# Kernel tuning notes

Hardware: AMD Instinct MI355X
Metric: run time of the kernel (lower is better)

The kernel has to match this reference:

```python
import jax, jax.numpy as jnp
import numpy as np

BATCH, SEQ, DIM = 256, 80, 1024
HEADS = 8
HID = 4 * DIM
EPS = 1e-5


def _ln(x, g, b):
    mu = jnp.mean(x, axis=-1, keepdims=True)
    var = jnp.mean((x - mu) ** 2, axis=-1, keepdims=True)
    return (x - mu) * jax.lax.rsqrt(var + EPS) * g + b


def setup_inputs() -> dict:
    key = jax.random.key(0)
    ks = jax.random.split(key, 8)
    w = lambda k, shape: jax.random.normal(k, shape, dtype=jnp.float32) * 0.02
    return {
        "x": jax.random.normal(ks[0], (BATCH, SEQ, DIM), dtype=jnp.float32),
        "Wq": w(ks[1], (DIM, DIM)),
        "Wk": w(ks[2], (DIM, DIM)),
        "Wv": w(ks[3], (DIM, DIM)),
        "bias_table": w(ks[4], (2 * SEQ - 1, HEADS)),
        "to_out_g": jnp.ones((DIM,), jnp.float32),
        "to_out_b": jnp.zeros((DIM,), jnp.float32),
        "ln1_g": jnp.ones((DIM,), jnp.float32),
        "ln1_b": jnp.zeros((DIM,), jnp.float32),
        "ln2_g": jnp.ones((DIM,), jnp.float32),
        "ln2_b": jnp.zeros((DIM,), jnp.float32),
        "fc1_w": w(ks[5], (DIM, HID)),
        "fc1_b": jnp.zeros((HID,), jnp.float32),
        "fc2_w": w(ks[6], (HID, DIM)),
        "fc2_b": jnp.zeros((DIM,), jnp.float32),
    }


def reference(x, Wq, Wk, Wv, bias_table, to_out_g, to_out_b,
              ln1_g, ln1_b, ln2_g, ln2_b, fc1_w, fc1_b, fc2_w, fc2_b):
    B, S, E = x.shape
    H = HEADS
    D = E // H
    scale = E ** (-0.5)  # NOTE: full emb_size scale, faithful to source

    q = (x @ Wq).reshape(B, S, H, D).transpose(0, 2, 1, 3)  # bhsd
    k = (x @ Wk).reshape(B, S, H, D).transpose(0, 2, 1, 3)
    v = (x @ Wv).reshape(B, S, H, D).transpose(0, 2, 1, 3)

    attn = jnp.einsum('bhqd,bhkd->bhqk', q, k) * scale
    attn = jax.nn.softmax(attn, axis=-1)

    # relative bias added AFTER softmax (non-standard, faithful)
    idx = jnp.arange(S)[:, None] - jnp.arange(S)[None, :] + (S - 1)  # [S,S] in [0,2S-2]
    bias = bias_table[idx].transpose(2, 0, 1)  # (H, S, S)
    attn = attn + bias[None]

    out = jnp.einsum('bhqk,bhkd->bhqd', attn, v)
    out = out.transpose(0, 2, 1, 3).reshape(B, S, E)
    out = _ln(out, to_out_g, to_out_b)  # LayerNorm inside attention (to_out)

    x = _ln(x + out, ln1_g, ln1_b)      # post-norm residual 1
    h = jax.nn.gelu(x @ fc1_w + fc1_b, approximate=False)  # torch nn.GELU exact
    ff = h @ fc2_w + fc2_b
    return _ln(x + ff, ln2_g, ln2_b)    # post-norm residual 2
```

## Files before the change

### kernel.cpp

```cpp
#include <hip/hip_runtime.h>
#include <stdint.h>

#define BATCH 256
#define SEQ   80
#define DIM   1024
#define HEADS 8
#define HDIM  128
#define HID   4096
#define NTOK  (BATCH * SEQ)

typedef unsigned short u16;
using short8_t = __attribute__((ext_vector_type(8))) short;
using f32x4    = __attribute__((ext_vector_type(4))) float;

__device__ __forceinline__ u16 f2bf(float f) {
  unsigned u = __float_as_uint(f);
  u += 0x7fffu + ((u >> 16) & 1u);
  return (u16)(u >> 16);
}
__device__ __forceinline__ float bf2f(u16 u) {
  return __uint_as_float(((unsigned)u) << 16);
}

__device__ __forceinline__ float gelu_exact(float v) {
  return 0.5f * v * (1.0f + erff(v * 0.70710678118654752f));
}

#define GLD16(gp, lp)                                                   \
  __builtin_amdgcn_global_load_lds(                                     \
      (__attribute__((address_space(1))) void*)(void*)(gp),             \
      (__attribute__((address_space(3))) void*)(void*)(lp), 16, 0, 0)

__global__ __launch_bounds__(256) void cast_bf16_kernel(
    const float* __restrict__ in, u16* __restrict__ out, int n4) {
  int i = blockIdx.x * 256 + threadIdx.x;
  int stride = gridDim.x * 256;
  for (; i < n4; i += stride) {
    float4 v = ((const float4*)in)[i];
    uint2 o;
    o.x = (unsigned)f2bf(v.x) | ((unsigned)f2bf(v.y) << 16);
    o.y = (unsigned)f2bf(v.z) | ((unsigned)f2bf(v.w) << 16);
    ((uint2*)out)[i] = o;
  }
}

__global__ __launch_bounds__(256) void transpose_cast_kernel(
    const float* __restrict__ in, u16* __restrict__ out, int R, int C) {
  __shared__ float tile[32][33];
  int c0 = blockIdx.x * 32, r0 = blockIdx.y * 32;
  for (int k = 0; k < 4; k++) {
    int i = threadIdx.y + k * 8;
    tile[i][threadIdx.x] = in[(size_t)(r0 + i) * C + c0 + threadIdx.x];
  }
  __syncthreads();
  for (int k = 0; k < 4; k++) {
    int i = threadIdx.y + k * 8;
    out[(size_t)(c0 + i) * R + r0 + threadIdx.x] = f2bf(tile[threadIdx.x][i]);
  }
}

template <int EPI>
__global__ __launch_bounds__(512, 2) void gemm256(
    const u16* __restrict__ A, const u16* __restrict__ Bt,
    const float* __restrict__ bias, u16* __restrict__ outp,
    int M, int N, int K, int ntn) {
  __shared__ __align__(16) u16 lds[65536];

  const int tid  = threadIdx.x;
  const int lane = tid & 63, wave = tid >> 6;
  const int wm = wave >> 2, wn = wave & 3;
  const int lo = lane & 15, hi = lane >> 4;

  const int nwg = gridDim.x;
  {
  }
  int q8 = nwg >> 3, r8 = nwg & 7;
  int xcd = blockIdx.x & 7, off = blockIdx.x >> 3;
  int swz = (xcd < r8 ? xcd * (q8 + 1) : r8 * (q8 + 1) + (xcd - r8) * q8) + off;
  const int bn = swz % ntn;
  const int bm = swz / ntn;
  const size_t arow0 = (size_t)bm * 256;
  const size_t bcol0 = (size_t)bn * 256;

  const int prow = tid >> 2;
  const int lb = (tid & 3) ^ ((tid >> 3) & 3);
  const u16* srcA = A + (arow0 + prow) * K + lb * 8;
  const u16* srcB = Bt + (bcol0 + prow) * K + lb * 8;
  const size_t jstep = 128 * (size_t)K;

  u16* ldsA0 = lds + wave * 512;
  u16* ldsA1 = lds + 4096 + wave * 512;
  u16* ldsB0 = lds + 8192 + wave * 512;
  u16* ldsB1 = lds + 12288 + wave * 512;

  const int blk = hi ^ ((lo >> 1) & 3);
  const int abase = (wm * 128 + lo) * 32 + blk * 8;
  const int bbase = 8192 + (wn * 64 + lo) * 32 + blk * 8;

  f32x4 acc[8][4] = {};
  const int NT = K >> 5;

#pragma unroll
  for (int tt = 0; tt < 3; ++tt) {
    const u16* sa = srcA + (size_t)tt * 32;
    const u16* sb = srcB + (size_t)tt * 32;
    GLD16(sa, ldsA0 + tt * 16384);
    GLD16(sa + jstep, ldsA1 + tt * 16384);
    GLD16(sb, ldsB0 + tt * 16384);
    GLD16(sb + jstep, ldsB1 + tt * 16384);
  }
  asm volatile("s_waitcnt vmcnt(8)" ::: "memory");
  asm volatile("s_barrier" ::: "memory");

#define PHASES(T, DO_STAGE, VMASM)                                             \
  do {                                                                         \
    const int bufb = ((T) & 3) * 16384;                                        \
    short8_t a0[4], b0[4], a1[4];                                              \
    _Pragma("unroll") for (int m = 0; m < 4; ++m)                              \
        a0[m] = *(const short8_t*)&lds[bufb + abase + m * 512];                \
    _Pragma("unroll") for (int n = 0; n < 4; ++n)                              \
        b0[n] = *(const short8_t*)&lds[bufb + bbase + n * 512];                \
    if (DO_STAGE) {                                                            \
      const u16* sa = srcA + (size_t)((T) + 3) * 32;                           \
      GLD16(sa, ldsA0 + (((T) + 3) & 3) * 16384);                              \
      GLD16(sa + jstep, ldsA1 + (((T) + 3) & 3) * 16384);                      \
    }                                                                          \
    asm volatile("s_barrier" ::: "memory");                                    \
    __builtin_amdgcn_s_setprio(1);                                             \
    _Pragma("unroll") for (int m = 0; m < 4; ++m)                              \
        _Pragma("unroll") for (int n = 0; n < 4; ++n)                          \
            acc[m][n] = __builtin_amdgcn_mfma_f32_16x16x32_bf16(               \
                a0[m], b0[n], acc[m][n], 0, 0, 0);                             \
    __builtin_amdgcn_s_setprio(0);                                             \
    asm volatile("s_barrier" ::: "memory");                                    \
    _Pragma("unroll") for (int m = 0; m < 4; ++m)                              \
        a1[m] = *(const short8_t*)&lds[bufb + abase + (4 + m) * 512];          \
    if (DO_STAGE) {                                                            \
      const u16* sb = srcB + (size_t)((T) + 3) * 32;                           \
      GLD16(sb, ldsB0 + (((T) + 3) & 3) * 16384);                              \
      GLD16(sb + jstep, ldsB1 + (((T) + 3) & 3) * 16384);                      \
    }                                                                          \
    asm volatile("s_barrier" ::: "memory");                                    \
    __builtin_amdgcn_s_setprio(1);                                             \
    _Pragma("unroll") for (int m = 0; m < 4; ++m)                              \
        _Pragma("unroll") for (int n = 0; n < 4; ++n)                          \
            acc[4 + m][n] = __builtin_amdgcn_mfma_f32_16x16x32_bf16(           \
                a1[m], b0[n], acc[4 + m][n], 0, 0, 0);                         \
    __builtin_amdgcn_s_setprio(0);                                             \
    asm volatile(VMASM ::: "memory");                                          \
    asm volatile("s_barrier" ::: "memory");                                    \
  } while (0)

  for (int t = 0; t < NT - 3; ++t) PHASES(t, 1, "s_waitcnt vmcnt(8)");
  PHASES(NT - 3, 0, "s_waitcnt vmcnt(4)");
  PHASES(NT - 2, 0, "s_waitcnt vmcnt(0)");
  PHASES(NT - 1, 0, "");
#undef PHASES

  const size_t crow0 = arow0 + wm * 128;
  const int ccol0 = (int)bcol0 + wn * 64;
#pragma unroll
  for (int n = 0; n < 4; ++n) {
    int col = ccol0 + n * 16 + lo;
    float bv = 0.f;
    if constexpr (EPI != 0) bv = bias[col];
#pragma unroll
    for (int m = 0; m < 8; ++m) {
#pragma unroll
      for (int j = 0; j < 4; ++j) {
        size_t row = crow0 + m * 16 + hi * 4 + j;
        float v = acc[m][n][j] + bv;
        if constexpr (EPI == 1) v = gelu_exact(v);
        outp[row * N + col] = f2bf(v);
      }
    }
  }
}

__global__ __launch_bounds__(64) void attn_kernel(
    const u16* __restrict__ QKV, const float* __restrict__ bias_table,
    u16* __restrict__ attnout) {
  __shared__ __align__(16) u16 Kt[80 * 128];
  __shared__ __align__(16) u16 Vt[96 * 128];
  __shared__ float bias_l[159];

  const int bh = blockIdx.x;
  const int b = bh >> 3, h = bh & 7;
  const int lane = threadIdx.x, lo = lane & 15, hi = lane >> 4;
  const size_t tokbase = (size_t)b * SEQ * 3072;
  const u16* Qg = QKV + tokbase + h * HDIM;
  const u16* Kg = QKV + tokbase + 1024 + h * HDIM;
  const u16* Vg = QKV + tokbase + 2048 + h * HDIM;

#pragma unroll
  for (int i = 0; i < 20; i++) {
    int flat = i * 64 + lane;
    int row = flat >> 4;
    int col = (flat & 15) * 8;
    GLD16(Kg + (size_t)row * 3072 + col, &Kt[i * 512]);
    GLD16(Vg + (size_t)row * 3072 + col, &Vt[i * 512]);
  }
  for (int i = lane; i < 16 * 128; i += 64) Vt[80 * 128 + i] = 0;
  for (int i = lane; i < 159; i += 64) bias_l[i] = bias_table[i * 8 + h];
  asm volatile("s_waitcnt vmcnt(0)" ::: "memory");
  __syncthreads();

  f32x4 sa[5][5] = {};
#pragma unroll
  for (int ks = 0; ks < 4; ks++) {
    short8_t ak[5], bq[5];
#pragma unroll
    for (int m = 0; m < 5; m++)
      ak[m] = *(const short8_t*)&Kt[(m * 16 + lo) * 128 + ks * 32 + hi * 8];
#pragma unroll
    for (int n = 0; n < 5; n++)
      bq[n] = *(const short8_t*)(Qg + (size_t)(n * 16 + lo) * 3072 + ks * 32 + hi * 8);
#pragma unroll
    for (int m = 0; m < 5; m++)
#pragma unroll
      for (int n = 0; n < 5; n++)
        sa[m][n] = __builtin_amdgcn_mfma_f32_16x16x32_bf16(ak[m], bq[n], sa[m][n], 0, 0, 0);
  }
  __syncthreads();

  u16* p_lds = Kt;
  for (int i = lane; i < 80 * 16; i += 64) {
    int q = i >> 4, c = 80 + (i & 15);
    p_lds[q * 104 + c] = 0;
  }
  const float scale = 0.03125f;
#pragma unroll
  for (int n = 0; n < 5; n++) {
    float mx = -1e30f;
#pragma unroll
    for (int m = 0; m < 5; m++)
#pragma unroll
      for (int j = 0; j < 4; j++) {
        sa[m][n][j] *= scale;
        mx = fmaxf(mx, sa[m][n][j]);
      }
    mx = fmaxf(mx, __shfl_xor(mx, 16));
    mx = fmaxf(mx, __shfl_xor(mx, 32));
    float sm = 0.f;
#pragma unroll
    for (int m = 0; m < 5; m++)
#pragma unroll
      for (int j = 0; j < 4; j++) {
        float e = __expf(sa[m][n][j] - mx);
        sa[m][n][j] = e;
        sm += e;
      }
    sm += __shfl_xor(sm, 16);
    sm += __shfl_xor(sm, 32);
    float inv = 1.0f / sm;
    int q = n * 16 + lo;
#pragma unroll
    for (int m = 0; m < 5; m++)
#pragma unroll
      for (int j = 0; j < 4; j++) {
        int key = m * 16 + hi * 4 + j;
        float pv = sa[m][n][j] * inv + bias_l[q - key + 79];
        p_lds[q * 104 + key] = f2bf(pv);
      }
  }
  __syncthreads();

#pragma unroll
  for (int half = 0; half < 2; half++) {
    f32x4 oa[5][4] = {};
#pragma unroll
    for (int ks = 0; ks < 3; ks++) {
      short8_t ap[5];
#pragma unroll
      for (int m = 0; m < 5; m++)
        ap[m] = *(const short8_t*)&p_lds[(m * 16 + lo) * 104 + ks * 32 + hi * 8];
      short8_t bv[4];
#pragma unroll
      for (int nd = 0; nd < 4; nd++) {
        int d = (half * 4 + nd) * 16 + lo;
        short8_t tt;
#pragma unroll
        for (int j = 0; j < 8; j++)
          tt[j] = (short)Vt[(ks * 32 + hi * 8 + j) * 128 + d];
        bv[nd] = tt;
      }
#pragma unroll
      for (int m = 0; m < 5; m++)
#pragma unroll
        for (int nd = 0; nd < 4; nd++)
          oa[m][nd] = __builtin_amdgcn_mfma_f32_16x16x32_bf16(ap[m], bv[nd], oa[m][nd], 0, 0, 0);
    }
#pragma unroll
    for (int m = 0; m < 5; m++)
#pragma unroll
      for (int nd = 0; nd < 4; nd++)
#pragma unroll
        for (int j = 0; j < 4; j++) {
          int q = m * 16 + hi * 4 + j;
          int d = (half * 4 + nd) * 16 + lo;
          attnout[((size_t)b * SEQ + q) * DIM + h * HDIM + d] = f2bf(oa[m][nd][j]);
        }
  }
}

__device__ __forceinline__ void block_reduce2(float& a, float& b, float* sbuf) {
#pragma unroll
  for (int m = 1; m < 64; m <<= 1) {
    a += __shfl_xor(a, m);
    b += __shfl_xor(b, m);
  }
  int w = threadIdx.x >> 6;
  if ((threadIdx.x & 63) == 0) { sbuf[w * 2] = a; sbuf[w * 2 + 1] = b; }
  __syncthreads();
  a = sbuf[0] + sbuf[2] + sbuf[4] + sbuf[6];
  b = sbuf[1] + sbuf[3] + sbuf[5] + sbuf[7];
  __syncthreads();
}

__global__ __launch_bounds__(256) void fuse1_kernel(
    const u16* __restrict__ attnout, const float* __restrict__ x,
    const float* __restrict__ og, const float* __restrict__ ob,
    const float* __restrict__ g1, const float* __restrict__ b1,
    u16* __restrict__ x1b) {
  __shared__ float sbuf[8];
  const size_t base = (size_t)blockIdx.x * DIM;
  float a[4], r[4];
  float s0 = 0.f, s1 = 0.f;
#pragma unroll
  for (int i = 0; i < 4; i++) {
    int idx = threadIdx.x + i * 256;
    a[i] = bf2f(attnout[base + idx]);
    s0 += a[i];
    s1 += a[i] * a[i];
  }
  block_reduce2(s0, s1, sbuf);
  float mu = s0 * (1.f / DIM);
  float rstd = rsqrtf(s1 * (1.f / DIM) - mu * mu + 1e-5f);
  float t0 = 0.f, t1 = 0.f;
#pragma unroll
  for (int i = 0; i < 4; i++) {
    int idx = threadIdx.x + i * 256;
    float o = (a[i] - mu) * rstd * og[idx] + ob[idx];
    r[i] = x[base + idx] + o;
    t0 += r[i];
    t1 += r[i] * r[i];
  }
  block_reduce2(t0, t1, sbuf);
  float mu2 = t0 * (1.f / DIM);
  float rstd2 = rsqrtf(t1 * (1.f / DIM) - mu2 * mu2 + 1e-5f);
#pragma unroll
  for (int i = 0; i < 4; i++) {
    int idx = threadIdx.x + i * 256;
    x1b[base + idx] = f2bf((r[i] - mu2) * rstd2 * g1[idx] + b1[idx]);
  }
}

__global__ __launch_bounds__(256) void fuse2_kernel(
    const u16* __restrict__ x1b, const u16* __restrict__ ff,
    const float* __restrict__ g2, const float* __restrict__ b2,
    float* __restrict__ out) {
  __shared__ float sbuf[8];
  const size_t base = (size_t)blockIdx.x * DIM;
  float r[4];
  float s0 = 0.f, s1 = 0.f;
#pragma unroll
  for (int i = 0; i < 4; i++) {
    int idx = threadIdx.x + i * 256;
    r[i] = bf2f(x1b[base + idx]) + bf2f(ff[base + idx]);
    s0 += r[i];
    s1 += r[i] * r[i];
  }
  block_reduce2(s0, s1, sbuf);
  float mu = s0 * (1.f / DIM);
  float rstd = rsqrtf(s1 * (1.f / DIM) - mu * mu + 1e-5f);
#pragma unroll
  for (int i = 0; i < 4; i++) {
    int idx = threadIdx.x + i * 256;
    out[base + idx] = (r[i] - mu) * rstd * g2[idx] + b2[idx];
  }
}

extern "C" void kernel_launch(void* const* d_in, const int* in_sizes, int n_in,
                              void* d_out, int out_size, void* d_ws, size_t ws_size,
                              hipStream_t stream) {
  const float* x        = (const float*)d_in[0];
  const float* Wq       = (const float*)d_in[1];
  const float* Wk       = (const float*)d_in[2];
  const float* Wv       = (const float*)d_in[3];
  const float* bias_tab = (const float*)d_in[4];
  const float* og       = (const float*)d_in[5];
  const float* ob       = (const float*)d_in[6];
  const float* g1       = (const float*)d_in[7];
  const float* b1       = (const float*)d_in[8];
  const float* g2       = (const float*)d_in[9];
  const float* b2       = (const float*)d_in[10];
  const float* fc1w     = (const float*)d_in[11];
  const float* fc1b     = (const float*)d_in[12];
  const float* fc2w     = (const float*)d_in[13];
  const float* fc2b     = (const float*)d_in[14];

  char* ws = (char*)d_ws;
  u16* wqkvT = (u16*)(ws + 0);
  u16* fc1T  = (u16*)(ws + 6291456ull);
  u16* fc2T  = (u16*)(ws + 14680064ull);
  u16* pbuf  = (u16*)(ws + 23068672ull);
  u16* qbuf  = (u16*)(ws + 65011712ull);
  char* cbuf = ws + 106954752ull;
  size_t cavail = ws_size > 106954752ull ? ws_size - 106954752ull : 0;

  int cb = 1;
  while (cb < 16 && (size_t)(BATCH / cb) * SEQ * 3072 * 2 > cavail) cb <<= 1;
  int cf = 1;
  while (cf < 16 && (size_t)(NTOK / cf) * HID * 2 > cavail) cf <<= 1;

  dim3 tb(32, 8);
  cast_bf16_kernel<<<2048, 256, 0, stream>>>(x, qbuf, NTOK * DIM / 4);
  transpose_cast_kernel<<<dim3(32, 32), tb, 0, stream>>>(Wq, wqkvT, 1024, 1024);
  transpose_cast_kernel<<<dim3(32, 32), tb, 0, stream>>>(Wk, wqkvT + 1024 * 1024, 1024, 1024);
  transpose_cast_kernel<<<dim3(32, 32), tb, 0, stream>>>(Wv, wqkvT + 2 * 1024 * 1024, 1024, 1024);
  transpose_cast_kernel<<<dim3(128, 32), tb, 0, stream>>>(fc1w, fc1T, 1024, 4096);
  transpose_cast_kernel<<<dim3(32, 128), tb, 0, stream>>>(fc2w, fc2T, 4096, 1024);

  {
    const int nb = BATCH / cb;
    const int rows = nb * SEQ;
    u16* qkvc = (u16*)cbuf;
    const int nwg = (rows / 256) * (3072 / 256);
    for (int c = 0; c < cb; ++c) {
      const u16* xb_c = qbuf + (size_t)c * rows * DIM;
      gemm256<0><<<nwg, 512, 0, stream>>>(xb_c, wqkvT, nullptr, qkvc,
                                          rows, 3072, 1024, 3072 / 256);
      attn_kernel<<<nb * HEADS, 64, 0, stream>>>(
          qkvc, bias_tab, pbuf + (size_t)c * rows * DIM);
    }
  }

  fuse1_kernel<<<NTOK, 256, 0, stream>>>(pbuf, x, og, ob, g1, b1, qbuf);

  {
    const int rows = NTOK / cf;
    u16* hc = (u16*)cbuf;
    const int nwg1 = (rows / 256) * (HID / 256);
    const int nwg2 = (rows / 256) * (DIM / 256);
    for (int c = 0; c < cf; ++c) {
      gemm256<1><<<nwg1, 512, 0, stream>>>(qbuf + (size_t)c * rows * DIM, fc1T,
                                           fc1b, hc, rows, HID, 1024, HID / 256);
      gemm256<2><<<nwg2, 512, 0, stream>>>(hc, fc2T, fc2b,
                                           pbuf + (size_t)c * rows * DIM,
                                           rows, 1024, HID, DIM / 256);
    }
  }

  fuse2_kernel<<<NTOK, 256, 0, stream>>>(qbuf, pbuf, g2, b2, (float*)d_out);
}
```

Measured before the change: 818.0 us.

## Switch GEMM to 32x32x16 MFMA, single barrier per K-step, LDS-staged epilogue

```diff
diff --git a/kernel.cpp b/kernel.cpp
--- a/kernel.cpp
+++ b/kernel.cpp
@@ -12,6 +12,7 @@
 typedef unsigned short u16;
 using short8_t = __attribute__((ext_vector_type(8))) short;
 using f32x4    = __attribute__((ext_vector_type(4))) float;
+using f32x16   = __attribute__((ext_vector_type(16))) float;
 
 __device__ __forceinline__ u16 f2bf(float f) {
   unsigned u = __float_as_uint(f);
@@ -69,11 +70,9 @@
   const int tid  = threadIdx.x;
   const int lane = tid & 63, wave = tid >> 6;
   const int wm = wave >> 2, wn = wave & 3;
-  const int lo = lane & 15, hi = lane >> 4;
+  const int l31 = lane & 31, khalf = lane >> 5;
 
   const int nwg = gridDim.x;
-  {
-  }
   int q8 = nwg >> 3, r8 = nwg & 7;
   int xcd = blockIdx.x & 7, off = blockIdx.x >> 3;
   int swz = (xcd < r8 ? xcd * (q8 + 1) : r8 * (q8 + 1) + (xcd - r8) * q8) + off;
@@ -88,92 +87,86 @@
   const u16* srcB = Bt + (bcol0 + prow) * K + lb * 8;
   const size_t jstep = 128 * (size_t)K;
 
-  u16* ldsA0 = lds + wave * 512;
-  u16* ldsA1 = lds + 4096 + wave * 512;
-  u16* ldsB0 = lds + 8192 + wave * 512;
-  u16* ldsB1 = lds + 12288 + wave * 512;
-
-  const int blk = hi ^ ((lo >> 1) & 3);
-  const int abase = (wm * 128 + lo) * 32 + blk * 8;
-  const int bbase = 8192 + (wn * 64 + lo) * 32 + blk * 8;
-
-  f32x4 acc[8][4] = {};
+  const int ar = wm * 128 + l31;
+  const int ab0 = ar * 32 + ((khalf ^ ((ar >> 1) & 3)) << 3);
+  const int bc = wn * 64 + l31;
+  const int bb0 = 8192 + bc * 32 + ((khalf ^ ((bc >> 1) & 3)) << 3);
+
+  f32x16 acc[4][2] = {};
   const int NT = K >> 5;
 
-#pragma unroll
-  for (int tt = 0; tt < 3; ++tt) {
-    const u16* sa = srcA + (size_t)tt * 32;
-    const u16* sb = srcB + (size_t)tt * 32;
-    GLD16(sa, ldsA0 + tt * 16384);
-    GLD16(sa + jstep, ldsA1 + tt * 16384);
-    GLD16(sb, ldsB0 + tt * 16384);
-    GLD16(sb + jstep, ldsB1 + tt * 16384);
-  }
+#define STAGE(u)                                                           \
+  do {                                                                     \
+    const u16* sa_ = srcA + (size_t)(u) * 32;                              \
+    const u16* sb_ = srcB + (size_t)(u) * 32;                              \
+    const int so_ = ((u) & 3) * 16384;                                     \
+    GLD16(sa_, lds + so_ + wave * 512);                                    \
+    GLD16(sa_ + jstep, lds + so_ + 4096 + wave * 512);                     \
+    GLD16(sb_, lds + so_ + 8192 + wave * 512);                             \
+    GLD16(sb_ + jstep, lds + so_ + 12288 + wave * 512);                    \
+  } while (0)
+
+#define ITER(t, DO_STAGE, VMASM)                                           \
+  do {                                                                     \
+    const int bo_ = ((t) & 3) * 16384;                                     \
+    short8_t af[4][2], bf[2][2];                                           \
+    _Pragma("unroll") for (int mi = 0; mi < 4; ++mi) {                     \
+      af[mi][0] = *(const short8_t*)&lds[(bo_ + ab0) + mi * 1024];         \
+      af[mi][1] = *(const short8_t*)&lds[((bo_ + ab0) ^ 16) + mi * 1024];  \
+    }                                                                      \
+    _Pragma("unroll") for (int ni = 0; ni < 2; ++ni) {                     \
+      bf[ni][0] = *(const short8_t*)&lds[(bo_ + bb0) + ni * 1024];         \
+      bf[ni][1] = *(const short8_t*)&lds[((bo_ + bb0) ^ 16) + ni * 1024];  \
+    }                                                                      \
+    if (DO_STAGE) STAGE((t) + 3);                                          \
+    __builtin_amdgcn_s_setprio(1);                                         \
+    _Pragma("unroll") for (int ks = 0; ks < 2; ++ks)                       \
+    _Pragma("unroll") for (int mi = 0; mi < 4; ++mi)                       \
+    _Pragma("unroll") for (int ni = 0; ni < 2; ++ni)                       \
+        acc[mi][ni] = __builtin_amdgcn_mfma_f32_32x32x16_bf16(             \
+            af[mi][ks], bf[ni][ks], acc[mi][ni], 0, 0, 0);                 \
+    __builtin_amdgcn_s_setprio(0);                                         \
+    asm volatile(VMASM ::: "memory");                                      \
+    asm volatile("s_barrier" ::: "memory");                                \
+  } while (0)
+
+#pragma unroll
+  for (int u = 0; u < 3; ++u) STAGE(u);
   asm volatile("s_waitcnt vmcnt(8)" ::: "memory");
   asm volatile("s_barrier" ::: "memory");
 
-#define PHASES(T, DO_STAGE, VMASM)                                             \
-  do {                                                                         \
-    const int bufb = ((T) & 3) * 16384;                                        \
-    short8_t a0[4], b0[4], a1[4];                                              \
-    _Pragma("unroll") for (int m = 0; m < 4; ++m)                              \
-        a0[m] = *(const short8_t*)&lds[bufb + abase + m * 512];                \
-    _Pragma("unroll") for (int n = 0; n < 4; ++n)                              \
-        b0[n] = *(const short8_t*)&lds[bufb + bbase + n * 512];                \
-    if (DO_STAGE) {                                                            \
-      const u16* sa = srcA + (size_t)((T) + 3) * 32;                           \
-      GLD16(sa, ldsA0 + (((T) + 3) & 3) * 16384);                              \
-      GLD16(sa + jstep, ldsA1 + (((T) + 3) & 3) * 16384);                      \
-    }                                                                          \
-    asm volatile("s_barrier" ::: "memory");                                    \
-    __builtin_amdgcn_s_setprio(1);                                             \
-    _Pragma("unroll") for (int m = 0; m < 4; ++m)                              \
-        _Pragma("unroll") for (int n = 0; n < 4; ++n)                          \
-            acc[m][n] = __builtin_amdgcn_mfma_f32_16x16x32_bf16(               \
-                a0[m], b0[n], acc[m][n], 0, 0, 0);                             \
-    __builtin_amdgcn_s_setprio(0);                                             \
-    asm volatile("s_barrier" ::: "memory");                                    \
-    _Pragma("unroll") for (int m = 0; m < 4; ++m)                              \
-        a1[m] = *(const short8_t*)&lds[bufb + abase + (4 + m) * 512];          \
-    if (DO_STAGE) {                                                            \
-      const u16* sb = srcB + (size_t)((T) + 3) * 32;                           \
-      GLD16(sb, ldsB0 + (((T) + 3) & 3) * 16384);                              \
-      GLD16(sb + jstep, ldsB1 + (((T) + 3) & 3) * 16384);                      \
-    }                                                                          \
-    asm volatile("s_barrier" ::: "memory");                                    \
-    __builtin_amdgcn_s_setprio(1);                                             \
-    _Pragma("unroll") for (int m = 0; m < 4; ++m)                              \
-        _Pragma("unroll") for (int n = 0; n < 4; ++n)                          \
-            acc[4 + m][n] = __builtin_amdgcn_mfma_f32_16x16x32_bf16(           \
-                a1[m], b0[n], acc[4 + m][n], 0, 0, 0);                         \
-    __builtin_amdgcn_s_setprio(0);                                             \
-    asm volatile(VMASM ::: "memory");                                          \
-    asm volatile("s_barrier" ::: "memory");                                    \
-  } while (0)
-
-  for (int t = 0; t < NT - 3; ++t) PHASES(t, 1, "s_waitcnt vmcnt(8)");
-  PHASES(NT - 3, 0, "s_waitcnt vmcnt(4)");
-  PHASES(NT - 2, 0, "s_waitcnt vmcnt(0)");
-  PHASES(NT - 1, 0, "");
-#undef PHASES
-
-  const size_t crow0 = arow0 + wm * 128;
-  const int ccol0 = (int)bcol0 + wn * 64;
-#pragma unroll
-  for (int n = 0; n < 4; ++n) {
-    int col = ccol0 + n * 16 + lo;
+#pragma unroll 4
+  for (int t = 0; t < NT - 3; ++t) ITER(t, 1, "s_waitcnt vmcnt(8)");
+  ITER(NT - 3, 0, "s_waitcnt vmcnt(4)");
+  ITER(NT - 2, 0, "s_waitcnt vmcnt(0)");
+  ITER(NT - 1, 0, "");
+#undef ITER
+#undef STAGE
+
+  u16* ct = lds;
+#pragma unroll
+  for (int ni = 0; ni < 2; ++ni) {
+    int col = wn * 64 + ni * 32 + l31;
     float bv = 0.f;
-    if constexpr (EPI != 0) bv = bias[col];
-#pragma unroll
-    for (int m = 0; m < 8; ++m) {
-#pragma unroll
-      for (int j = 0; j < 4; ++j) {
-        size_t row = crow0 + m * 16 + hi * 4 + j;
-        float v = acc[m][n][j] + bv;
+    if constexpr (EPI != 0) bv = bias[bcol0 + col];
+#pragma unroll
+    for (int mi = 0; mi < 4; ++mi) {
+#pragma unroll
+      for (int r = 0; r < 16; ++r) {
+        int row = wm * 128 + mi * 32 + (r & 3) + ((r >> 2) << 3) + (khalf << 2);
+        float v = acc[mi][ni][r] + bv;
         if constexpr (EPI == 1) v = gelu_exact(v);
-        outp[row * N + col] = f2bf(v);
+        ct[row * 256 + col] = f2bf(v);
       }
     }
+  }
+  __syncthreads();
+  u16* op = outp + arow0 * (size_t)N + bcol0;
+#pragma unroll
+  for (int i = 0; i < 16; ++i) {
+    int c = i * 512 + tid;
+    int row = c >> 5, o2 = (c & 31) * 8;
+    *(short8_t*)(op + (size_t)row * N + o2) = *(const short8_t*)&ct[row * 256 + o2];
   }
 }
 
```

Result: slower. 843.6 us (+3.1%).
